# Kernel optimization log

Hardware: AMD Instinct MI355X
Metric: run time of the kernel (lower is better)

Reference implementation:

```python
import math
import jax, jax.numpy as jnp
import numpy as np

N_HEADS = 16


def setup_inputs() -> dict:
    key = jax.random.key(0)
    k1, k2 = jax.random.split(key)
    # qkv: [N, H*C, T] queries; y: [N, H*C, S] keys/values (k = v = y)
    qkv = jax.random.normal(k1, (2, 1024, 2048), dtype=jnp.float32)
    y = jax.random.normal(k2, (2, 1024, 2048), dtype=jnp.float32)
    return {"qkv": qkv, "y": y}


def reference(qkv, y):
    bs, width, length = qkv.shape
    ch = width // N_HEADS  # head dim = 64
    q = qkv.reshape(bs * N_HEADS, ch, length)          # [B*H, C, T]
    k = v = y.reshape(bs * N_HEADS, ch, -1)            # [B*H, C, S]
    scale = 1.0 / math.sqrt(math.sqrt(ch))             # applied to both q and k
    weight = jnp.einsum('bct,bcs->bts', q * scale, k * scale)  # [B*H, T, S]
    weight = jax.nn.softmax(weight.astype(jnp.float32), axis=-1).astype(weight.dtype)
    a = jnp.einsum('bts,bcs->bct', weight, v)          # [B*H, C, T]
    return a.reshape(bs, -1, length)                   # [N, H*C, T]
```

## Files before the change

### kernel.cpp

```cpp
#include <hip/hip_runtime.h>
#include <hip/hip_bf16.h>


typedef __attribute__((ext_vector_type(4))) float f32x4;
typedef __attribute__((ext_vector_type(8))) short bf16x8;
typedef __attribute__((ext_vector_type(4))) float float4_t;
typedef __attribute__((ext_vector_type(4))) unsigned u32x4;

__device__ __forceinline__ unsigned short f2bf(float f) {
  unsigned u = __builtin_bit_cast(unsigned, f);
  u += 0x7FFFu + ((u >> 16) & 1u);
  return (unsigned short)(u >> 16);
}

#if __has_builtin(__builtin_amdgcn_exp2f)
#define EXP2F(x) __builtin_amdgcn_exp2f(x)
#else
#define EXP2F(x) __expf((x) * 0.6931471805599453f)
#endif

__device__ __forceinline__ unsigned pack_bf2(float a, float b) {
  unsigned short lo = __builtin_bit_cast(unsigned short, __float2bfloat16(a));
  unsigned short hi = __builtin_bit_cast(unsigned short, __float2bfloat16(b));
  return (unsigned)lo | ((unsigned)hi << 16);
}

#define GLOAD_LDS16(g, l) __builtin_amdgcn_global_load_lds(                 \
    (const __attribute__((address_space(1))) unsigned*)(g),                 \
    (__attribute__((address_space(3))) unsigned*)(l), 16, 0, 0)

#define SCL (0.35355339059327373f * 1.2011224087864498f)

__global__ __launch_bounds__(256)
void prep(const float* __restrict__ qkv, const float* __restrict__ y,
          unsigned short* __restrict__ kT, unsigned short* __restrict__ v,
          unsigned short* __restrict__ qT) {
  __shared__ unsigned short tb[64][66];
  const int tid = threadIdx.x;
  const int isQ = blockIdx.x >> 10;
  const int b2  = blockIdx.x & 1023;
  const int bh  = b2 >> 5;
  const int s0  = (b2 & 31) * 64;
  const float* src = (isQ ? qkv : y) + (size_t)bh * 131072;

  const int c = tid >> 2, j = tid & 3;
  float fv[16];
  #pragma unroll
  for (int p = 0; p < 4; ++p) {
    float4_t a = *(const float4_t*)(src + c * 2048 + s0 + j * 16 + p * 4);
    #pragma unroll
    for (int i = 0; i < 4; ++i) fv[p * 4 + i] = a[i];
  }
  if (!isQ) {
    bf16x8 u0, u1;
    #pragma unroll
    for (int i = 0; i < 8; ++i) { u0[i] = (short)f2bf(fv[i]); u1[i] = (short)f2bf(fv[8 + i]); }
    unsigned short* vp = v + (size_t)bh * 131072 + c * 2048 + s0 + j * 16;
    *(bf16x8*)(vp) = u0;
    *(bf16x8*)(vp + 8) = u1;
  }
  #pragma unroll
  for (int m = 0; m < 8; ++m) {
    unsigned lo = f2bf(fv[2 * m] * SCL);
    unsigned hi = f2bf(fv[2 * m + 1] * SCL);
    *(unsigned*)&tb[c][j * 16 + 2 * m] = lo | (hi << 16);
  }
  __syncthreads();

  const int srow = tid >> 2, i2 = tid & 3;
  unsigned short outv[16];
  #pragma unroll
  for (int m = 0; m < 16; ++m) outv[m] = tb[i2 * 16 + m][srow];
  unsigned short* dT = (isQ ? qT : kT) + (size_t)bh * 131072 +
                       (size_t)(s0 + srow) * 64 + i2 * 16;
  *(bf16x8*)(dT)     = *(bf16x8*)&outv[0];
  *(bf16x8*)(dT + 8) = *(bf16x8*)&outv[8];
}

#define KOFF0 0
#define KOFF1 8192
#define VOFF0 16384
#define VOFF1 24576
#define LDS_MAIN 32768

__global__ __launch_bounds__(512, 2)
void attn_main(const unsigned short* __restrict__ kT,
               const unsigned short* __restrict__ v,
               const unsigned short* __restrict__ qT,
               float* __restrict__ out) {
  __shared__ __align__(16) char smem[LDS_MAIN];
  const int tid  = threadIdx.x;
  const int lane = tid & 63;
  const int w    = tid >> 6;
  const int c15  = lane & 15;
  const int g    = lane >> 4;

  const int bid = blockIdx.x;
  const int bh  = (bid & 7) * 4 + ((bid >> 3) & 3);
  const int t0  = (bid >> 5) * 256;

  const unsigned short* kg = kT + (size_t)bh * 131072;
  const unsigned short* vg = v  + (size_t)bh * 131072;
  float*                og = out + (size_t)bh * 131072;

  bf16x8 qf[2][2];
  {
    const unsigned short* qp0 = qT + (size_t)bh * 131072 +
                                (size_t)(t0 + w * 32 + c15) * 64 + 8 * g;
    qf[0][0] = *(const bf16x8*)(qp0);
    qf[0][1] = *(const bf16x8*)(qp0 + 32);
    qf[1][0] = *(const bf16x8*)(qp0 + 1024);
    qf[1][1] = *(const bf16x8*)(qp0 + 1024 + 32);
  }

  const int sr = tid >> 3, sb = tid & 7;
  const int ss = sb ^ (sr & 7);
  const unsigned short* kbase = kg + sr * 64 + ss * 8;
  const unsigned short* vbase = vg + sr * 2048 + ss * 8;
  char* const slds = smem + tid * 16;

  f32x4 oacc[2][4];
  #pragma unroll
  for (int tg = 0; tg < 2; ++tg)
    #pragma unroll
    for (int nc = 0; nc < 4; ++nc) oacc[tg][nc] = (f32x4){0.f, 0.f, 0.f, 0.f};
  float lsum[2] = {0.f, 0.f};

  GLOAD_LDS16(kbase, slds + KOFF0);
  GLOAD_LDS16(vbase, slds + VOFF0);
  __syncthreads();

  auto tile = [&](int koff, int voff, int nkoff, int nvoff, int it) {
    if (it + 1 < 32) {
      GLOAD_LDS16(kbase + (it + 1) * 4096, slds + nkoff);
      GLOAD_LDS16(vbase + (it + 1) * 64,   slds + nvoff);
    }
    char* kb = smem + koff;
    char* vb = smem + voff;

    f32x4 acc[2][4];
    #pragma unroll
    for (int tg = 0; tg < 2; ++tg)
      #pragma unroll
      for (int nt = 0; nt < 4; ++nt) acc[tg][nt] = (f32x4){0.f, 0.f, 0.f, 0.f};
    #pragma unroll
    for (int kt = 0; kt < 2; ++kt)
      #pragma unroll
      for (int nt = 0; nt < 4; ++nt) {
        const int srow = nt * 16 + c15;
        bf16x8 kf = *(bf16x8*)(kb + srow * 128 + (((kt * 4 + g) ^ (srow & 7)) * 16));
        acc[0][nt] = __builtin_amdgcn_mfma_f32_16x16x32_bf16(kf, qf[0][kt], acc[0][nt], 0, 0, 0);
        acc[1][nt] = __builtin_amdgcn_mfma_f32_16x16x32_bf16(kf, qf[1][kt], acc[1][nt], 0, 0, 0);
      }

    bf16x8 pa[2][2];
    #pragma unroll
    for (int tg = 0; tg < 2; ++tg) {
      unsigned W[8];
      #pragma unroll
      for (int nt = 0; nt < 4; ++nt) {
        float p0 = EXP2F(acc[tg][nt][0]);
        float p1 = EXP2F(acc[tg][nt][1]);
        float p2 = EXP2F(acc[tg][nt][2]);
        float p3 = EXP2F(acc[tg][nt][3]);
        lsum[tg] += (p0 + p1) + (p2 + p3);
        W[nt * 2]     = pack_bf2(p0, p1);
        W[nt * 2 + 1] = pack_bf2(p2, p3);
      }
      #pragma unroll
      for (int kt = 0; kt < 2; ++kt) {
        unsigned a0 = W[kt * 4 + 0], b0 = W[kt * 4 + 2];
        unsigned a1 = W[kt * 4 + 1], b1 = W[kt * 4 + 3];
        asm volatile("v_permlane32_swap_b32 %0, %1" : "+v"(a0), "+v"(b0));
        asm volatile("v_permlane32_swap_b32 %0, %1" : "+v"(a1), "+v"(b1));
        asm volatile("v_permlane16_swap_b32 %0, %1" : "+v"(a0), "+v"(b0));
        asm volatile("v_permlane16_swap_b32 %0, %1" : "+v"(a1), "+v"(b1));
        u32x4 fw = {a0, a1, b0, b1};
        pa[tg][kt] = __builtin_bit_cast(bf16x8, fw);
      }
    }

    #pragma unroll
    for (int kt = 0; kt < 2; ++kt)
      #pragma unroll
      for (int nc = 0; nc < 4; ++nc) {
        const int crow = nc * 16 + c15;
        bf16x8 vf = *(bf16x8*)(vb + crow * 128 + (((kt * 4 + g) ^ (crow & 7)) * 16));
        oacc[0][nc] = __builtin_amdgcn_mfma_f32_16x16x32_bf16(vf, pa[0][kt], oacc[0][nc], 0, 0, 0);
        oacc[1][nc] = __builtin_amdgcn_mfma_f32_16x16x32_bf16(vf, pa[1][kt], oacc[1][nc], 0, 0, 0);
      }
    __syncthreads();
  };

  #pragma unroll 1
  for (int it2 = 0; it2 < 16; ++it2) {
    tile(KOFF0, VOFF0, KOFF1, VOFF1, 2 * it2);
    tile(KOFF1, VOFF1, KOFF0, VOFF0, 2 * it2 + 1);
  }

  #pragma unroll
  for (int tg = 0; tg < 2; ++tg) {
    lsum[tg] += __shfl_xor(lsum[tg], 16);
    lsum[tg] += __shfl_xor(lsum[tg], 32);
  }
  const float invl0 = 1.0f / lsum[0];
  const float invl1 = 1.0f / lsum[1];

  float* ob = og + t0 + w * 32 + c15 + (size_t)(4 * g) * 2048;
  #pragma unroll
  for (int nc = 0; nc < 4; ++nc)
    #pragma unroll
    for (int r = 0; r < 4; ++r) {
      ob[(size_t)(nc * 16 + r) * 2048]      = oacc[0][nc][r] * invl0;
      ob[(size_t)(nc * 16 + r) * 2048 + 16] = oacc[1][nc][r] * invl1;
    }
}

#define LDS_K 0
#define LDS_V 8192
#define LDS_P 16384
#define LDS_TOTAL 27648

__global__ __launch_bounds__(256)
void attn_fwd(const float* __restrict__ qkv, const float* __restrict__ y,
              float* __restrict__ out) {
  __shared__ __align__(16) char smem[LDS_TOTAL];
  const int tid  = threadIdx.x;
  const int lane = tid & 63;
  const int w    = tid >> 6;
  const int c15  = lane & 15;
  const int g    = lane >> 4;
  const int bh = blockIdx.x >> 5;
  const int t0 = (blockIdx.x & 31) * 64;
  const float* qg = qkv + (size_t)bh * 64 * 2048;
  const float* kg = y   + (size_t)bh * 64 * 2048;
  float*       og = out + (size_t)bh * 64 * 2048;
  const float SC = 0.35355339059327373f;
  bf16x8 qf[2];
  {
    const int tq = t0 + w * 16 + c15;
    #pragma unroll
    for (int kt = 0; kt < 2; ++kt)
      #pragma unroll
      for (int j = 0; j < 8; ++j)
        qf[kt][j] = (short)f2bf(qg[(kt * 32 + 8 * g + j) * 2048 + tq] * SC);
  }
  f32x4 oacc[4];
  #pragma unroll
  for (int nc = 0; nc < 4; ++nc) oacc[nc] = (f32x4){0.f, 0.f, 0.f, 0.f};
  float m_run[4], l_run[4];
  #pragma unroll
  for (int r = 0; r < 4; ++r) { m_run[r] = -1e30f; l_run[r] = 0.f; }
  const int ks_row = tid & 63, ks_cb = tid >> 6;
  const int vs_c = tid >> 2, vs_j = tid & 3;
  for (int it = 0; it < 32; ++it) {
    const int s0 = it * 64;
    #pragma unroll
    for (int pass = 0; pass < 2; ++pass) {
      const int cblk = pass * 4 + ks_cb;
      bf16x8 pk;
      #pragma unroll
      for (int i = 0; i < 8; ++i)
        pk[i] = (short)f2bf(kg[(cblk * 8 + i) * 2048 + s0 + ks_row] * SC);
      *(bf16x8*)(smem + LDS_K + ks_row * 128 + ((cblk ^ (ks_row & 7)) * 16)) = pk;
    }
    #pragma unroll
    for (int pass = 0; pass < 2; ++pass) {
      const int sblk = pass * 4 + vs_j;
      const float4_t a = *(const float4_t*)(kg + vs_c * 2048 + s0 + sblk * 8);
      const float4_t b = *(const float4_t*)(kg + vs_c * 2048 + s0 + sblk * 8 + 4);
      bf16x8 pv;
      #pragma unroll
      for (int i = 0; i < 4; ++i) { pv[i] = (short)f2bf(a[i]); pv[4 + i] = (short)f2bf(b[i]); }
      *(bf16x8*)(smem + LDS_V + vs_c * 128 + ((sblk ^ (vs_c & 7)) * 16)) = pv;
    }
    __syncthreads();
    f32x4 accs[4];
    #pragma unroll
    for (int nt = 0; nt < 4; ++nt) accs[nt] = (f32x4){0.f, 0.f, 0.f, 0.f};
    #pragma unroll
    for (int kt = 0; kt < 2; ++kt)
      #pragma unroll
      for (int nt = 0; nt < 4; ++nt) {
        const int srow = nt * 16 + c15;
        bf16x8 kf = *(bf16x8*)(smem + LDS_K + srow * 128 +
                               (((kt * 4 + g) ^ (srow & 7)) * 16));
        accs[nt] = __builtin_amdgcn_mfma_f32_16x16x32_bf16(qf[kt], kf, accs[nt], 0, 0, 0);
      }
    float mt[4];
    #pragma unroll
    for (int r = 0; r < 4; ++r)
      mt[r] = fmaxf(fmaxf(accs[0][r], accs[1][r]), fmaxf(accs[2][r], accs[3][r]));
    #pragma unroll
    for (int off = 1; off <= 8; off <<= 1)
      #pragma unroll
      for (int r = 0; r < 4; ++r) mt[r] = fmaxf(mt[r], __shfl_xor(mt[r], off));
    float alpha[4];
    #pragma unroll
    for (int r = 0; r < 4; ++r) {
      float mn = fmaxf(m_run[r], mt[r]);
      alpha[r] = __expf(m_run[r] - mn);
      m_run[r] = mn;
    }
    float ls[4] = {0.f, 0.f, 0.f, 0.f};
    #pragma unroll
    for (int nt = 0; nt < 4; ++nt)
      #pragma unroll
      for (int r = 0; r < 4; ++r) {
        float p = __expf(accs[nt][r] - m_run[r]);
        accs[nt][r] = p;
        ls[r] += p;
      }
    #pragma unroll
    for (int off = 1; off <= 8; off <<= 1)
      #pragma unroll
      for (int r = 0; r < 4; ++r) ls[r] += __shfl_xor(ls[r], off);
    #pragma unroll
    for (int r = 0; r < 4; ++r) l_run[r] = l_run[r] * alpha[r] + ls[r];
    #pragma unroll
    for (int nc = 0; nc < 4; ++nc)
      #pragma unroll
      for (int r = 0; r < 4; ++r) oacc[nc][r] *= alpha[r];
    char* pb = smem + LDS_P + w * 2816;
    #pragma unroll
    for (int nt = 0; nt < 4; ++nt)
      #pragma unroll
      for (int r = 0; r < 4; ++r)
        *(unsigned short*)(pb + (4 * g + r) * 176 + (nt * 16 + c15) * 2) =
            f2bf(accs[nt][r]);
    __builtin_amdgcn_sched_barrier(0);
    #pragma unroll
    for (int kt = 0; kt < 2; ++kt) {
      bf16x8 pf = *(bf16x8*)(pb + c15 * 176 + (kt * 32 + 8 * g) * 2);
      #pragma unroll
      for (int nc = 0; nc < 4; ++nc) {
        const int crow = nc * 16 + c15;
        bf16x8 vf = *(bf16x8*)(smem + LDS_V + crow * 128 +
                               (((kt * 4 + g) ^ (crow & 7)) * 16));
        oacc[nc] = __builtin_amdgcn_mfma_f32_16x16x32_bf16(pf, vf, oacc[nc], 0, 0, 0);
      }
    }
    __syncthreads();
  }
  float inv_l[4];
  #pragma unroll
  for (int r = 0; r < 4; ++r) inv_l[r] = 1.0f / l_run[r];
  float* ep = (float*)smem;
  #pragma unroll
  for (int nc = 0; nc < 4; ++nc)
    #pragma unroll
    for (int r = 0; r < 4; ++r)
      ep[(nc * 16 + c15) * 68 + (w * 16 + 4 * g + r)] = oacc[nc][r] * inv_l[r];
  __syncthreads();
  #pragma unroll
  for (int itr = 0; itr < 4; ++itr) {
    int idx = itr * 256 + tid;
    int cc  = idx >> 4;
    int v4  = idx & 15;
    float4_t o = *(float4_t*)(ep + cc * 68 + v4 * 4);
    *(float4_t*)(og + cc * 2048 + t0 + v4 * 4) = o;
  }
}

extern "C" void kernel_launch(void* const* d_in, const int* in_sizes, int n_in,
                              void* d_out, int out_size, void* d_ws, size_t ws_size,
                              hipStream_t stream) {
  const float* qkv = (const float*)d_in[0];
  const float* y   = (const float*)d_in[1];
  float*       out = (float*)d_out;
  if (ws_size < (size_t)25165824) {
    attn_fwd<<<dim3(1024), dim3(256), 0, stream>>>(qkv, y, out);
    return;
  }
  unsigned short* kT = (unsigned short*)d_ws;
  unsigned short* vv = kT + 4194304;
  unsigned short* qT = kT + 8388608;
  prep<<<dim3(2048), dim3(256), 0, stream>>>(qkv, y, kT, vv, qT);
  attn_main<<<dim3(256), dim3(512), 0, stream>>>(kT, vv, qT, out);
}
```

Measured before the change: 60.27 us.

## Double-buffer 128-key windows with interleaved softmax/MFMA and priority hints

The attention main loop now processes 128 keys per barrier window instead of 64, with two 32KB LDS buffers, so it takes half as many barriers. Softmax of the first half overlaps with the PV MFMAs of the second, steered by s_setprio hints and sched_barrier. The exp2 and bf16 packing now use the single hardware instructions v_exp_f32 and v_cvt_pk_bf16_f32 through inline asm. LDS per block doubles to 64KB, which may limit occupancy at two blocks per CU, and an explicit vmcnt(0) wait precedes each window.

```diff
diff --git a/kernel.cpp b/kernel.cpp
--- a/kernel.cpp
+++ b/kernel.cpp
@@ -13,16 +13,16 @@
   return (unsigned short)(u >> 16);
 }
 
-#if __has_builtin(__builtin_amdgcn_exp2f)
-#define EXP2F(x) __builtin_amdgcn_exp2f(x)
-#else
-#define EXP2F(x) __expf((x) * 0.6931471805599453f)
-#endif
-
-__device__ __forceinline__ unsigned pack_bf2(float a, float b) {
-  unsigned short lo = __builtin_bit_cast(unsigned short, __float2bfloat16(a));
-  unsigned short hi = __builtin_bit_cast(unsigned short, __float2bfloat16(b));
-  return (unsigned)lo | ((unsigned)hi << 16);
+__device__ __forceinline__ float exp2_fast(float x) {
+  float r;
+  asm("v_exp_f32 %0, %1" : "=v"(r) : "v"(x));
+  return r;
+}
+
+__device__ __forceinline__ unsigned cvt_pk_bf16(float a, float b) {
+  unsigned r;
+  asm("v_cvt_pk_bf16_f32 %0, %1, %2" : "=v"(r) : "v"(a), "v"(b));
+  return r;
 }
 
 #define GLOAD_LDS16(g, l) __builtin_amdgcn_global_load_lds(                 \
@@ -77,18 +77,14 @@
   *(bf16x8*)(dT + 8) = *(bf16x8*)&outv[8];
 }
 
-#define KOFF0 0
-#define KOFF1 8192
-#define VOFF0 16384
-#define VOFF1 24576
-#define LDS_MAIN 32768
+#define WBS 32768
 
 __global__ __launch_bounds__(512, 2)
 void attn_main(const unsigned short* __restrict__ kT,
                const unsigned short* __restrict__ v,
                const unsigned short* __restrict__ qT,
                float* __restrict__ out) {
-  __shared__ __align__(16) char smem[LDS_MAIN];
+  __shared__ __align__(16) char smem[2 * WBS];
   const int tid  = threadIdx.x;
   const int lane = tid & 63;
   const int w    = tid >> 6;
@@ -126,23 +122,7 @@
     for (int nc = 0; nc < 4; ++nc) oacc[tg][nc] = (f32x4){0.f, 0.f, 0.f, 0.f};
   float lsum[2] = {0.f, 0.f};
 
-  GLOAD_LDS16(kbase, slds + KOFF0);
-  GLOAD_LDS16(vbase, slds + VOFF0);
-  __syncthreads();
-
-  auto tile = [&](int koff, int voff, int nkoff, int nvoff, int it) {
-    if (it + 1 < 32) {
-      GLOAD_LDS16(kbase + (it + 1) * 4096, slds + nkoff);
-      GLOAD_LDS16(vbase + (it + 1) * 64,   slds + nvoff);
-    }
-    char* kb = smem + koff;
-    char* vb = smem + voff;
-
-    f32x4 acc[2][4];
-    #pragma unroll
-    for (int tg = 0; tg < 2; ++tg)
-      #pragma unroll
-      for (int nt = 0; nt < 4; ++nt) acc[tg][nt] = (f32x4){0.f, 0.f, 0.f, 0.f};
+  auto QK = [&](f32x4 (&acc)[2][4], char* kb) {
     #pragma unroll
     for (int kt = 0; kt < 2; ++kt)
       #pragma unroll
@@ -152,20 +132,20 @@
         acc[0][nt] = __builtin_amdgcn_mfma_f32_16x16x32_bf16(kf, qf[0][kt], acc[0][nt], 0, 0, 0);
         acc[1][nt] = __builtin_amdgcn_mfma_f32_16x16x32_bf16(kf, qf[1][kt], acc[1][nt], 0, 0, 0);
       }
-
-    bf16x8 pa[2][2];
+  };
+  auto SM = [&](f32x4 (&acc)[2][4], bf16x8 (&pa)[2][2]) {
     #pragma unroll
     for (int tg = 0; tg < 2; ++tg) {
       unsigned W[8];
       #pragma unroll
       for (int nt = 0; nt < 4; ++nt) {
-        float p0 = EXP2F(acc[tg][nt][0]);
-        float p1 = EXP2F(acc[tg][nt][1]);
-        float p2 = EXP2F(acc[tg][nt][2]);
-        float p3 = EXP2F(acc[tg][nt][3]);
+        float p0 = exp2_fast(acc[tg][nt][0]);
+        float p1 = exp2_fast(acc[tg][nt][1]);
+        float p2 = exp2_fast(acc[tg][nt][2]);
+        float p3 = exp2_fast(acc[tg][nt][3]);
         lsum[tg] += (p0 + p1) + (p2 + p3);
-        W[nt * 2]     = pack_bf2(p0, p1);
-        W[nt * 2 + 1] = pack_bf2(p2, p3);
+        W[nt * 2]     = cvt_pk_bf16(p0, p1);
+        W[nt * 2 + 1] = cvt_pk_bf16(p2, p3);
       }
       #pragma unroll
       for (int kt = 0; kt < 2; ++kt) {
@@ -179,7 +159,8 @@
         pa[tg][kt] = __builtin_bit_cast(bf16x8, fw);
       }
     }
-
+  };
+  auto PV = [&](bf16x8 (&pa)[2][2], char* vb) {
     #pragma unroll
     for (int kt = 0; kt < 2; ++kt)
       #pragma unroll
@@ -189,13 +170,56 @@
         oacc[0][nc] = __builtin_amdgcn_mfma_f32_16x16x32_bf16(vf, pa[0][kt], oacc[0][nc], 0, 0, 0);
         oacc[1][nc] = __builtin_amdgcn_mfma_f32_16x16x32_bf16(vf, pa[1][kt], oacc[1][nc], 0, 0, 0);
       }
-    __syncthreads();
   };
 
+  auto window = [&](int bs, int wn, bool doIssue) {
+    asm volatile("s_waitcnt vmcnt(0)" ::: "memory");
+    __builtin_amdgcn_s_barrier();
+    __builtin_amdgcn_sched_barrier(0);
+    if (doIssue) {
+      const unsigned short* kp = kbase + (size_t)(wn + 1) * 8192;
+      const unsigned short* vp = vbase + (wn + 1) * 128;
+      char* const ob = slds + (bs ^ 1) * WBS;
+      GLOAD_LDS16(kp,        ob);
+      GLOAD_LDS16(kp + 4096, ob + 8192);
+      GLOAD_LDS16(vp,        ob + 16384);
+      GLOAD_LDS16(vp + 64,   ob + 24576);
+    }
+    __builtin_amdgcn_sched_barrier(0);
+
+    char* const base = smem + bs * WBS;
+    f32x4 accA[2][4], accB[2][4];
+    #pragma unroll
+    for (int tg = 0; tg < 2; ++tg)
+      #pragma unroll
+      for (int nt = 0; nt < 4; ++nt) {
+        accA[tg][nt] = (f32x4){0.f, 0.f, 0.f, 0.f};
+        accB[tg][nt] = (f32x4){0.f, 0.f, 0.f, 0.f};
+      }
+    __builtin_amdgcn_s_setprio(1);
+    QK(accA, base);
+    QK(accB, base + 8192);
+    __builtin_amdgcn_s_setprio(0);
+    bf16x8 paA[2][2], paB[2][2];
+    SM(accA, paA);
+    __builtin_amdgcn_s_setprio(1);
+    PV(paA, base + 16384);
+    __builtin_amdgcn_s_setprio(0);
+    SM(accB, paB);
+    __builtin_amdgcn_s_setprio(1);
+    PV(paB, base + 24576);
+    __builtin_amdgcn_s_setprio(0);
+  };
+
+  GLOAD_LDS16(kbase,        slds);
+  GLOAD_LDS16(kbase + 4096, slds + 8192);
+  GLOAD_LDS16(vbase,        slds + 16384);
+  GLOAD_LDS16(vbase + 64,   slds + 24576);
+
   #pragma unroll 1
-  for (int it2 = 0; it2 < 16; ++it2) {
-    tile(KOFF0, VOFF0, KOFF1, VOFF1, 2 * it2);
-    tile(KOFF1, VOFF1, KOFF0, VOFF0, 2 * it2 + 1);
+  for (int mi = 0; mi < 8; ++mi) {
+    window(0, 2 * mi,     true);
+    window(1, 2 * mi + 1, mi < 7);
   }
 
   #pragma unroll
@@ -236,6 +260,7 @@
   const float* kg = y   + (size_t)bh * 64 * 2048;
   float*       og = out + (size_t)bh * 64 * 2048;
   const float SC = 0.35355339059327373f;
+  typedef __attribute__((ext_vector_type(4))) float f4;
   bf16x8 qf[2];
   {
     const int tq = t0 + w * 16 + c15;
@@ -267,8 +292,8 @@
     #pragma unroll
     for (int pass = 0; pass < 2; ++pass) {
       const int sblk = pass * 4 + vs_j;
-      const float4_t a = *(const float4_t*)(kg + vs_c * 2048 + s0 + sblk * 8);
-      const float4_t b = *(const float4_t*)(kg + vs_c * 2048 + s0 + sblk * 8 + 4);
+      const f4 a = *(const f4*)(kg + vs_c * 2048 + s0 + sblk * 8);
+      const f4 b = *(const f4*)(kg + vs_c * 2048 + s0 + sblk * 8 + 4);
       bf16x8 pv;
       #pragma unroll
       for (int i = 0; i < 4; ++i) { pv[i] = (short)f2bf(a[i]); pv[4 + i] = (short)f2bf(b[i]); }
@@ -357,8 +382,8 @@
     int idx = itr * 256 + tid;
     int cc  = idx >> 4;
     int v4  = idx & 15;
-    float4_t o = *(float4_t*)(ep + cc * 68 + v4 * 4);
-    *(float4_t*)(og + cc * 2048 + t0 + v4 * 4) = o;
+    f4 o = *(f4*)(ep + cc * 68 + v4 * 4);
+    *(f4*)(og + cc * 2048 + t0 + v4 * 4) = o;
   }
 }
 
```

Result: faster. 53.49 us, median of 3 (-11.3%).
